# Kernel optimization log

Measured on AMD Instinct MI355X. Metric: run time of the kernel, lower is better.

The kernel has to match this reference:

```python
import jax, jax.numpy as jnp
import numpy as np

# --- config (matches init_kwargs) ---
E = 32          # n_routed_experts
G = 8           # n_group
TKG = 4         # topk_group
K = 4           # num_experts_per_tok
D = 2048        # hidden_size
H = 1024        # moe_intermediate_size
HS = 4096       # moe_shared_expert_intermediate_size
SCALE = 2.5     # routed_scaling_factor
CAP = 1024


def setup_inputs() -> dict:
    key = jax.random.key(0)
    ks = jax.random.split(key, 6)
    B, S = 2, 2048
    return dict(
        hidden_states=jax.random.normal(ks[0], (B, S, D), jnp.float32),
        gate_w=jax.random.normal(ks[1], (E, D), jnp.float32) * 0.02,
        bias_corr=jnp.zeros((E,), jnp.float32),  # e_score_correction_bias
        up_w=jax.random.normal(ks[2], (E, H, D), jnp.float32) * 0.02,
        down_w=jax.random.normal(ks[3], (E, D, H), jnp.float32) * 0.02,
        shared_up_w=jax.random.normal(ks[4], (HS, D), jnp.float32) * 0.02,
        shared_down_w=jax.random.normal(ks[5], (D, HS), jnp.float32) * 0.02,
    )


def relu2(x):
    r = jnp.maximum(x, 0.0)
    return r * r


def route_tokens(scores, bias_corr):
    # scores: sigmoid(router_logits), [T, E]
    T = scores.shape[0]
    scores_c = scores + bias_corr                                  # for choice
    group_scores = jax.lax.top_k(scores_c.reshape(T, G, E // G), 2)[0].sum(-1)  # [T, G]
    _, group_idx = jax.lax.top_k(group_scores, TKG)                # [T, TKG]
    group_mask = jnp.zeros((T, G), scores.dtype).at[jnp.arange(T)[:, None], group_idx].set(1.0)
    score_mask = jnp.repeat(group_mask, E // G, axis=1)            # [T, E]
    masked = jnp.where(score_mask > 0, scores_c, 0.0)
    _, topk_idx = jax.lax.top_k(masked, K)                         # [T, K]
    topk_w = jnp.take_along_axis(scores, topk_idx, axis=1)         # weights from raw sigmoid scores
    topk_w = topk_w / (topk_w.sum(-1, keepdims=True) + 1e-20)      # norm_topk_prob
    return topk_idx, topk_w * SCALE


def reference(hidden_states, gate_w, bias_corr, up_w, down_w, shared_up_w, shared_down_w):
    B, S, _ = hidden_states.shape
    T = B * S
    flat = hidden_states.reshape(T, D)

    logits = flat @ gate_w.T                                       # [T, E]
    scores = jax.nn.sigmoid(logits)
    topk_idx, topk_w = route_tokens(scores, bias_corr)             # [T, K] each

    # --- capacity-based dispatch (equivalent to per-expert gather + index_add combine) ---
    e_flat = topk_idx.reshape(-1)                                  # [T*K]
    oh = jax.nn.one_hot(e_flat, E, dtype=jnp.int32)                # [T*K, E]
    pos = jnp.take_along_axis(jnp.cumsum(oh, axis=0) - 1, e_flat[:, None], axis=1)[:, 0]
    tok = jnp.repeat(jnp.arange(T), K)                             # token idx per assignment
    valid = pos < CAP

    xe = jnp.zeros((E, CAP, D), flat.dtype).at[e_flat, pos].set(flat[tok], mode='drop')
    h = relu2(jnp.einsum('ecd,ehd->ech', xe, up_w))                # [E, CAP, H]
    ye = jnp.einsum('ech,edh->ecd', h, down_w)                     # [E, CAP, D]

    gathered = ye[e_flat, jnp.minimum(pos, CAP - 1)]               # [T*K, D]
    gathered = jnp.where(valid[:, None], gathered, 0.0) * topk_w.reshape(-1)[:, None]
    routed = gathered.reshape(T, K, D).sum(axis=1).reshape(B, S, D)

    shared = relu2(hidden_states @ shared_up_w.T) @ shared_down_w.T
    return routed + shared
```

## Files before the change

kernel.cpp:

```cpp
#include <hip/hip_runtime.h>

#define NE 32
#define NG 8
#define NK 4
#define ND 2048
#define NH 1024
#define NHS 4096
#define CAPE 1024
#define NT 4096

typedef float f32x4 __attribute__((ext_vector_type(4)));
typedef short s16x8 __attribute__((ext_vector_type(8)));

__device__ __forceinline__ short f2bf(float f) {
    return __builtin_bit_cast(short, (__bf16)f);
}
__device__ __forceinline__ float bf2f(short h) {
    return __builtin_bit_cast(float, ((unsigned)(unsigned short)h) << 16);
}

__device__ __forceinline__ void gload_lds16(const void* g, void* l) {
    __builtin_amdgcn_global_load_lds(
        (const __attribute__((address_space(1))) void*)g,
        (__attribute__((address_space(3))) void*)l, 16, 0, 0);
}

__global__ __launch_bounds__(256) void gate_kernel(
    const float* __restrict__ X, const float* __restrict__ Gw,
    const float* __restrict__ bias,
    int* __restrict__ topk_idx, float* __restrict__ topk_w)
{
    const int lane = threadIdx.x & 63;
    const int t = blockIdx.x * 4 + (threadIdx.x >> 6);
    const float* x = X + (size_t)t * ND;

    float xr[32];
#pragma unroll
    for (int i = 0; i < 32; i++) xr[i] = x[lane + i * 64];

    float scores[32];
#pragma unroll
    for (int e = 0; e < 32; e++) {
        const float* w = Gw + (size_t)e * ND;
        float a = 0.f;
#pragma unroll
        for (int i = 0; i < 32; i++) a = fmaf(xr[i], w[lane + i * 64], a);
#pragma unroll
        for (int s = 32; s > 0; s >>= 1) a += __shfl_xor(a, s);
        scores[e] = 1.0f / (1.0f + expf(-a));
    }

    float sc_c[32];
#pragma unroll
    for (int e = 0; e < 32; e++) sc_c[e] = scores[e] + bias[e];

    float gs[8];
#pragma unroll
    for (int g = 0; g < 8; g++) {
        float a = sc_c[4 * g], b = sc_c[4 * g + 1], c = sc_c[4 * g + 2], d = sc_c[4 * g + 3];
        float hi1 = fmaxf(a, b), lo1 = fminf(a, b);
        float hi2 = fmaxf(c, d), lo2 = fminf(c, d);
        float m1 = fmaxf(hi1, hi2);
        float m2 = fmaxf(fminf(hi1, hi2), fmaxf(lo1, lo2));
        gs[g] = m1 + m2;
    }

    unsigned gsel = 0;
#pragma unroll
    for (int it = 0; it < 4; it++) {
        int best = -1; float bv = -1e30f;
#pragma unroll
        for (int g = 0; g < 8; g++) {
            bool avail = !((gsel >> g) & 1);
            if (avail && gs[g] > bv) { bv = gs[g]; best = g; }
        }
        gsel |= 1u << best;
    }

    unsigned esel = 0;
    int idxs[4]; float wts[4];
#pragma unroll
    for (int it = 0; it < 4; it++) {
        int best = -1; float bv = -1e30f, braw = 0.f;
#pragma unroll
        for (int e = 0; e < 32; e++) {
            float mv = ((gsel >> (e >> 2)) & 1) ? sc_c[e] : 0.0f;
            bool avail = !((esel >> e) & 1);
            if (avail && mv > bv) { bv = mv; best = e; braw = scores[e]; }
        }
        esel |= 1u << best;
        idxs[it] = best; wts[it] = braw;
    }

    float s = wts[0] + wts[1] + wts[2] + wts[3] + 1e-20f;
    if (lane == 0) {
#pragma unroll
        for (int k = 0; k < 4; k++) {
            topk_idx[t * 4 + k] = idxs[k];
            topk_w[t * 4 + k] = wts[k] / s * 2.5f;
        }
    }
}

__global__ void zero_cnt(int* cnt) {
    if (threadIdx.x < NE) cnt[threadIdx.x] = 0;
}

__global__ void dispatch_kernel(const int* __restrict__ topk_idx,
                                int* __restrict__ cnt,
                                int* __restrict__ tok_list,
                                int* __restrict__ pos_list)
{
    int i = blockIdx.x * 256 + threadIdx.x;
    int e = topk_idx[i];
    int t = i >> 2;
    int pos = atomicAdd(&cnt[e], 1);
    pos_list[i] = pos;
    if (pos < CAPE) {
        tok_list[e * CAPE + pos] = t;
    }
}

__global__ __launch_bounds__(256) void cvt_f2bf(const float* __restrict__ in,
                                                short* __restrict__ out, int n8)
{
    int i = blockIdx.x * 256 + threadIdx.x;
    int stride = gridDim.x * 256;
    for (; i < n8; i += stride) {
        const f32x4* p = (const f32x4*)(in + (size_t)i * 8);
        f32x4 a = p[0], b = p[1];
        s16x8 h;
        h[0] = f2bf(a[0]); h[1] = f2bf(a[1]); h[2] = f2bf(a[2]); h[3] = f2bf(a[3]);
        h[4] = f2bf(b[0]); h[5] = f2bf(b[1]); h[6] = f2bf(b[2]); h[7] = f2bf(b[3]);
        *(s16x8*)(out + (size_t)i * 8) = h;
    }
}

__global__ __launch_bounds__(256) void combine_kernel(
    const int* __restrict__ topk_idx, const float* __restrict__ topk_w,
    const int* __restrict__ pos_list,
    const short* __restrict__ Ybuf, float* __restrict__ out)
{
    const int t = blockIdx.x;
    const int d0 = threadIdx.x * 8;

    int e[NK], p[NK]; float w[NK];
#pragma unroll
    for (int k = 0; k < NK; k++) {
        e[k] = topk_idx[t * NK + k];
        p[k] = pos_list[t * NK + k];
        w[k] = topk_w[t * NK + k];
    }

    float* orow = out + (size_t)t * ND + d0;
    f32x4 o0 = *(f32x4*)(orow);
    f32x4 o1 = *(f32x4*)(orow + 4);

#pragma unroll
    for (int k = 0; k < NK; k++) {
        if (p[k] < CAPE) {
            s16x8 y = *(const s16x8*)(Ybuf + ((size_t)e[k] * CAPE + p[k]) * ND + d0);
            o0[0] = fmaf(w[k], bf2f(y[0]), o0[0]);
            o0[1] = fmaf(w[k], bf2f(y[1]), o0[1]);
            o0[2] = fmaf(w[k], bf2f(y[2]), o0[2]);
            o0[3] = fmaf(w[k], bf2f(y[3]), o0[3]);
            o1[0] = fmaf(w[k], bf2f(y[4]), o1[0]);
            o1[1] = fmaf(w[k], bf2f(y[5]), o1[1]);
            o1[2] = fmaf(w[k], bf2f(y[6]), o1[2]);
            o1[3] = fmaf(w[k], bf2f(y[7]), o1[3]);
        }
    }
    *(f32x4*)(orow) = o0;
    *(f32x4*)(orow + 4) = o1;
}

template <int MODE, int BM, int BN>
__global__ __launch_bounds__(512, 2) void moe_gemm8(
    const short* __restrict__ Abase, const short* __restrict__ Bbase,
    const int* __restrict__ cnt, const int* __restrict__ tok_list,
    short* __restrict__ Hout, float* __restrict__ out)
{
    constexpr int K = (MODE == 0) ? ND : (MODE == 1) ? NH : (MODE == 2) ? ND : NHS;
    constexpr int NTILES = K / 64;
    constexpr int MF = BM / 32;
    constexpr int NF = BN / 64;
    constexpr int A_OPS = BM / 64;
    constexpr int B_OPS = BN / 64;
    constexpr int LOADS = A_OPS + B_OPS;

    const int e = blockIdx.z;
    const int m0 = blockIdx.y * BM, n0 = blockIdx.x * BN;

    int mcnt = 0;
    if constexpr (MODE == 0 || MODE == 1) {
        mcnt = min(cnt[e], CAPE);
        if (m0 >= mcnt) return;
    }

    __shared__ short As[2][BM * 64];
    __shared__ short Bs[2][BN * 64];

    const int tid = threadIdx.x;
    const int lane = tid & 63;
    const int wave = tid >> 6;
    const int wrM = wave >> 2;
    const int wrN = wave & 3;

    const short* Ab = Abase;
    const short* Bb = Bbase;
    if constexpr (MODE == 0) Bb += (size_t)e * NH * ND;
    if constexpr (MODE == 1) { Ab += (size_t)e * CAPE * NH; Bb += (size_t)e * ND * NH; }

    const int srow = tid >> 3;
    const int p = tid & 7;
    const int gcol = (p ^ (srow & 7)) * 8;
    const short* asrc[A_OPS];
    const short* bsrc[B_OPS];
    int dstA[A_OPS], dstB[B_OPS];
#pragma unroll
    for (int o = 0; o < A_OPS; o++) {
        int r = o * 64 + srow;
        if constexpr (MODE == 0) {
            int gr = min(m0 + r, mcnt - 1);
            int tok = tok_list[e * CAPE + gr];
            asrc[o] = Abase + (size_t)tok * ND + gcol;
        } else if constexpr (MODE == 1) {
            int gr = min(m0 + r, mcnt - 1);
            asrc[o] = Ab + (size_t)gr * NH + gcol;
        } else if constexpr (MODE == 2) {
            asrc[o] = Abase + (size_t)(m0 + r) * ND + gcol;
        } else {
            asrc[o] = Abase + (size_t)(m0 + r) * NHS + gcol;
        }
        dstA[o] = o * 4096 + wave * 512;
    }
#pragma unroll
    for (int o = 0; o < B_OPS; o++) {
        bsrc[o] = Bb + (size_t)(n0 + o * 64 + srow) * K + gcol;
        dstB[o] = o * 4096 + wave * 512;
    }

    auto STAGE = [&](int tt) {
        const int ko = (tt < NTILES ? tt : NTILES - 1) * 64;
        short* Ad = As[tt & 1];
        short* Bd = Bs[tt & 1];
#pragma unroll
        for (int o = 0; o < A_OPS; o++) gload_lds16(asrc[o] + ko, Ad + dstA[o]);
#pragma unroll
        for (int o = 0; o < B_OPS; o++) gload_lds16(bsrc[o] + ko, Bd + dstB[o]);
    };

    const int r16 = lane & 15, hi4 = lane >> 4, lo3 = lane & 7;
    const int physbase = (hi4 ^ lo3) * 8;
    int offA[MF], offB[NF];
#pragma unroll
    for (int m = 0; m < MF; m++)
        offA[m] = (wrM * (BM / 2) + m * 16 + r16) * 64 + physbase;
#pragma unroll
    for (int n = 0; n < NF; n++)
        offB[n] = (wrN * (BN / 4) + n * 16 + r16) * 64 + physbase;

    f32x4 acc[MF][NF] = {};

    STAGE(0);
    STAGE(1);

    for (int t = 0; t < NTILES; ++t) {
        const short* At = As[t & 1];
        const short* Bt = Bs[t & 1];
        if constexpr (LOADS == 6)
            asm volatile("s_waitcnt vmcnt(6)" ::: "memory");
        else if constexpr (LOADS == 8)
            asm volatile("s_waitcnt vmcnt(8)" ::: "memory");
        else
            asm volatile("s_waitcnt vmcnt(0)" ::: "memory");
        __builtin_amdgcn_s_barrier();
        __builtin_amdgcn_sched_barrier(0);
        s16x8 af[MF], bf[NF];
#pragma unroll
        for (int m = 0; m < MF; m++) af[m] = *(const s16x8*)(At + offA[m]);
#pragma unroll
        for (int n = 0; n < NF; n++) bf[n] = *(const s16x8*)(Bt + offB[n]);
        asm volatile("s_waitcnt lgkmcnt(0)" ::: "memory");
        __builtin_amdgcn_sched_barrier(0);
        __builtin_amdgcn_s_setprio(1);
#pragma unroll
        for (int m = 0; m < MF; m++)
#pragma unroll
            for (int n = 0; n < NF; n++)
                acc[m][n] = __builtin_amdgcn_mfma_f32_16x16x32_bf16(af[m], bf[n], acc[m][n], 0, 0, 0);
        __builtin_amdgcn_s_setprio(0);
        s16x8 ag[MF], bg[NF];
#pragma unroll
        for (int m = 0; m < MF; m++) ag[m] = *(const s16x8*)(At + (offA[m] ^ 32));
#pragma unroll
        for (int n = 0; n < NF; n++) bg[n] = *(const s16x8*)(Bt + (offB[n] ^ 32));
        asm volatile("s_waitcnt lgkmcnt(0)" ::: "memory");
        __builtin_amdgcn_sched_barrier(0);
        __builtin_amdgcn_s_barrier();
        __builtin_amdgcn_sched_barrier(0);
        STAGE(t + 2);
        __builtin_amdgcn_s_setprio(1);
#pragma unroll
        for (int m = 0; m < MF; m++)
#pragma unroll
            for (int n = 0; n < NF; n++)
                acc[m][n] = __builtin_amdgcn_mfma_f32_16x16x32_bf16(ag[m], bg[n], acc[m][n], 0, 0, 0);
        __builtin_amdgcn_s_setprio(0);
    }

    const int r0 = (lane >> 4) * 4;
    const int cc = lane & 15;

    if constexpr (MODE == 0 || MODE == 2) {
#pragma unroll
        for (int i = 0; i < MF; i++)
#pragma unroll
            for (int j = 0; j < NF; j++)
#pragma unroll
                for (int v = 0; v < 4; v++) {
                    int row = wrM * (BM / 2) + i * 16 + r0 + v;
                    int col = wrN * (BN / 4) + j * 16 + cc;
                    float val = acc[i][j][v];
                    float r = fmaxf(val, 0.f);
                    val = r * r;
                    if constexpr (MODE == 0)
                        Hout[((size_t)e * CAPE + m0 + row) * NH + (n0 + col)] = f2bf(val);
                    else
                        Hout[(size_t)(m0 + row) * NHS + (n0 + col)] = f2bf(val);
                }
    } else if constexpr (MODE == 3) {
#pragma unroll
        for (int i = 0; i < MF; i++)
#pragma unroll
            for (int j = 0; j < NF; j++)
#pragma unroll
                for (int v = 0; v < 4; v++) {
                    int row = wrM * (BM / 2) + i * 16 + r0 + v;
                    int col = wrN * (BN / 4) + j * 16 + cc;
                    out[(size_t)(m0 + row) * ND + (n0 + col)] = acc[i][j][v];
                }
    } else {
#pragma unroll
        for (int i = 0; i < MF; i++)
#pragma unroll
            for (int v = 0; v < 4; v++) {
                int row = wrM * (BM / 2) + i * 16 + r0 + v;
                int grow = m0 + row;
                if (grow < mcnt) {
#pragma unroll
                    for (int j = 0; j < NF; j++) {
                        int col = wrN * (BN / 4) + j * 16 + cc;
                        Hout[((size_t)e * CAPE + grow) * ND + (n0 + col)] = f2bf(acc[i][j][v]);
                    }
                }
            }
    }
}

extern "C" void kernel_launch(void* const* d_in, const int* in_sizes, int n_in,
                              void* d_out, int out_size, void* d_ws, size_t ws_size,
                              hipStream_t stream) {
    const float* X    = (const float*)d_in[0];
    const float* Gw   = (const float*)d_in[1];
    const float* bias = (const float*)d_in[2];
    const float* up_w = (const float*)d_in[3];
    const float* dn_w = (const float*)d_in[4];
    const float* sup  = (const float*)d_in[5];
    const float* sdn  = (const float*)d_in[6];
    float* out = (float*)d_out;

    char* ws = (char*)d_ws;
    size_t off = 0;
    auto alloc = [&](size_t bytes) -> void* {
        off = (off + 255) & ~(size_t)255;
        void* p = ws + off;
        off += bytes;
        return p;
    };
    int*   cnt      = (int*)  alloc(NE * 4);
    int*   topk_idx = (int*)  alloc((size_t)NT * NK * 4);
    float* topk_w   = (float*)alloc((size_t)NT * NK * 4);
    int*   pos_list = (int*)  alloc((size_t)NT * NK * 4);
    int*   tok_list = (int*)  alloc((size_t)NE * CAPE * 4);
    short* Hbuf     = (short*)alloc((size_t)NE * CAPE * NH * 2);
    short* Sbuf     = (short*)alloc((size_t)NT * NHS * 2);
    short* Xbf      = (short*)alloc((size_t)NT * ND * 2);
    short* up_bf    = (short*)alloc((size_t)NE * NH * ND * 2);
    short* dn_bf    = (short*)alloc((size_t)NE * ND * NH * 2);
    short* sup_bf   = (short*)alloc((size_t)NHS * ND * 2);
    short* sdn_bf   = (short*)alloc((size_t)ND * NHS * 2);
    short* Ybuf     = Xbf;

    gate_kernel<<<dim3(NT / 4), dim3(256), 0, stream>>>(X, Gw, bias, topk_idx, topk_w);
    zero_cnt<<<dim3(1), dim3(64), 0, stream>>>(cnt);
    dispatch_kernel<<<dim3(NT * NK / 256), dim3(256), 0, stream>>>(
        topk_idx, cnt, tok_list, pos_list);

    cvt_f2bf<<<dim3(1024), dim3(256), 0, stream>>>(X,    Xbf,    NT * ND / 8);
    cvt_f2bf<<<dim3(2048), dim3(256), 0, stream>>>(up_w, up_bf,  NE * NH * ND / 8);
    cvt_f2bf<<<dim3(2048), dim3(256), 0, stream>>>(dn_w, dn_bf,  NE * ND * NH / 8);
    cvt_f2bf<<<dim3(1024), dim3(256), 0, stream>>>(sup,  sup_bf, NHS * ND / 8);
    cvt_f2bf<<<dim3(1024), dim3(256), 0, stream>>>(sdn,  sdn_bf, ND * NHS / 8);

    moe_gemm8<0, 128, 256><<<dim3(NH / 256, CAPE / 128, NE), dim3(512), 0, stream>>>(
        Xbf, up_bf, cnt, tok_list, Hbuf, nullptr);
    moe_gemm8<2, 256, 256><<<dim3(NHS / 256, NT / 256, 1), dim3(512), 0, stream>>>(
        Xbf, sup_bf, nullptr, nullptr, Sbuf, nullptr);
    moe_gemm8<3, 256, 128><<<dim3(ND / 128, NT / 256, 1), dim3(512), 0, stream>>>(
        Sbuf, sdn_bf, nullptr, nullptr, nullptr, out);
    moe_gemm8<1, 128, 256><<<dim3(ND / 256, CAPE / 128, NE), dim3(512), 0, stream>>>(
        Hbuf, dn_bf, cnt, tok_list, Ybuf, nullptr);
    combine_kernel<<<dim3(NT), dim3(256), 0, stream>>>(
        topk_idx, topk_w, pos_list, Ybuf, out);
}
```

Measured before the change: 790.1 us.

## Use four-stage BK=32 LDS pipeline and 256-row tiles for expert GEMMs

Rewrites the GEMM main loop from a double-buffered K=64 tile with two barriers per iteration into a four-buffer ring of K=32 tiles. Loads run three stages ahead and each iteration needs only one barrier. The LDS swizzle is reworked for the 32-column row layout. The expert up/down GEMMs also move from 128-row to 256-row tiles, which halves the number of M blocks per expert. The intent is to hide more global-load latency and cut barrier overhead. In exchange, each iteration does less MFMA work, and the larger expert tiles waste more work on partially filled experts and may reduce occupancy.

```diff
diff --git a/kernel.cpp b/kernel.cpp
--- a/kernel.cpp
+++ b/kernel.cpp
@@ -181,11 +181,11 @@
     short* __restrict__ Hout, float* __restrict__ out)
 {
     constexpr int K = (MODE == 0) ? ND : (MODE == 1) ? NH : (MODE == 2) ? ND : NHS;
-    constexpr int NTILES = K / 64;
+    constexpr int NTILES = K / 32;
     constexpr int MF = BM / 32;
     constexpr int NF = BN / 64;
-    constexpr int A_OPS = BM / 64;
-    constexpr int B_OPS = BN / 64;
+    constexpr int A_OPS = BM / 128;
+    constexpr int B_OPS = BN / 128;
     constexpr int LOADS = A_OPS + B_OPS;
 
     const int e = blockIdx.z;
@@ -197,8 +197,8 @@
         if (m0 >= mcnt) return;
     }
 
-    __shared__ short As[2][BM * 64];
-    __shared__ short Bs[2][BN * 64];
+    __shared__ short As[4][BM * 32];
+    __shared__ short Bs[4][BN * 32];
 
     const int tid = threadIdx.x;
     const int lane = tid & 63;
@@ -211,15 +211,16 @@
     if constexpr (MODE == 0) Bb += (size_t)e * NH * ND;
     if constexpr (MODE == 1) { Ab += (size_t)e * CAPE * NH; Bb += (size_t)e * ND * NH; }
 
-    const int srow = tid >> 3;
-    const int p = tid & 7;
-    const int gcol = (p ^ (srow & 7)) * 8;
+    const int srow = tid >> 2;
+    const int p = tid & 3;
+    const int swzs = (srow ^ (srow >> 2)) & 3;
+    const int gcol = (p ^ swzs) * 8;
     const short* asrc[A_OPS];
     const short* bsrc[B_OPS];
     int dstA[A_OPS], dstB[B_OPS];
 #pragma unroll
     for (int o = 0; o < A_OPS; o++) {
-        int r = o * 64 + srow;
+        int r = o * 128 + srow;
         if constexpr (MODE == 0) {
             int gr = min(m0 + r, mcnt - 1);
             int tok = tok_list[e * CAPE + gr];
@@ -236,51 +237,58 @@
     }
 #pragma unroll
     for (int o = 0; o < B_OPS; o++) {
-        bsrc[o] = Bb + (size_t)(n0 + o * 64 + srow) * K + gcol;
+        bsrc[o] = Bb + (size_t)(n0 + o * 128 + srow) * K + gcol;
         dstB[o] = o * 4096 + wave * 512;
     }
 
     auto STAGE = [&](int tt) {
-        const int ko = (tt < NTILES ? tt : NTILES - 1) * 64;
-        short* Ad = As[tt & 1];
-        short* Bd = Bs[tt & 1];
+        const int ko = (tt < NTILES ? tt : NTILES - 1) * 32;
+        short* Ad = As[tt & 3];
+        short* Bd = Bs[tt & 3];
 #pragma unroll
         for (int o = 0; o < A_OPS; o++) gload_lds16(asrc[o] + ko, Ad + dstA[o]);
 #pragma unroll
         for (int o = 0; o < B_OPS; o++) gload_lds16(bsrc[o] + ko, Bd + dstB[o]);
     };
 
-    const int r16 = lane & 15, hi4 = lane >> 4, lo3 = lane & 7;
-    const int physbase = (hi4 ^ lo3) * 8;
+    const int r16 = lane & 15;
+    const int kslot = lane >> 4;
+    const int rswz = (r16 ^ (r16 >> 2)) & 3;
+    const int physcol = (kslot ^ rswz) * 8;
     int offA[MF], offB[NF];
 #pragma unroll
     for (int m = 0; m < MF; m++)
-        offA[m] = (wrM * (BM / 2) + m * 16 + r16) * 64 + physbase;
+        offA[m] = (wrM * (BM / 2) + m * 16 + r16) * 32 + physcol;
 #pragma unroll
     for (int n = 0; n < NF; n++)
-        offB[n] = (wrN * (BN / 4) + n * 16 + r16) * 64 + physbase;
+        offB[n] = (wrN * (BN / 4) + n * 16 + r16) * 32 + physcol;
 
     f32x4 acc[MF][NF] = {};
 
-    STAGE(0);
-    STAGE(1);
+    STAGE(0); STAGE(1); STAGE(2);
 
     for (int t = 0; t < NTILES; ++t) {
-        const short* At = As[t & 1];
-        const short* Bt = Bs[t & 1];
-        if constexpr (LOADS == 6)
+        const short* At = As[t & 3];
+        const short* Bt = Bs[t & 3];
+        if constexpr (LOADS == 4)
+            asm volatile("s_waitcnt vmcnt(8)" ::: "memory");
+        else if constexpr (LOADS == 3)
             asm volatile("s_waitcnt vmcnt(6)" ::: "memory");
-        else if constexpr (LOADS == 8)
-            asm volatile("s_waitcnt vmcnt(8)" ::: "memory");
+        else if constexpr (LOADS == 2)
+            asm volatile("s_waitcnt vmcnt(4)" ::: "memory");
         else
             asm volatile("s_waitcnt vmcnt(0)" ::: "memory");
         __builtin_amdgcn_s_barrier();
         __builtin_amdgcn_sched_barrier(0);
+
         s16x8 af[MF], bf[NF];
 #pragma unroll
         for (int m = 0; m < MF; m++) af[m] = *(const s16x8*)(At + offA[m]);
 #pragma unroll
         for (int n = 0; n < NF; n++) bf[n] = *(const s16x8*)(Bt + offB[n]);
+
+        STAGE(t + 3);
+
         asm volatile("s_waitcnt lgkmcnt(0)" ::: "memory");
         __builtin_amdgcn_sched_barrier(0);
         __builtin_amdgcn_s_setprio(1);
@@ -289,23 +297,6 @@
 #pragma unroll
             for (int n = 0; n < NF; n++)
                 acc[m][n] = __builtin_amdgcn_mfma_f32_16x16x32_bf16(af[m], bf[n], acc[m][n], 0, 0, 0);
-        __builtin_amdgcn_s_setprio(0);
-        s16x8 ag[MF], bg[NF];
-#pragma unroll
-        for (int m = 0; m < MF; m++) ag[m] = *(const s16x8*)(At + (offA[m] ^ 32));
-#pragma unroll
-        for (int n = 0; n < NF; n++) bg[n] = *(const s16x8*)(Bt + (offB[n] ^ 32));
-        asm volatile("s_waitcnt lgkmcnt(0)" ::: "memory");
-        __builtin_amdgcn_sched_barrier(0);
-        __builtin_amdgcn_s_barrier();
-        __builtin_amdgcn_sched_barrier(0);
-        STAGE(t + 2);
-        __builtin_amdgcn_s_setprio(1);
-#pragma unroll
-        for (int m = 0; m < MF; m++)
-#pragma unroll
-            for (int n = 0; n < NF; n++)
-                acc[m][n] = __builtin_amdgcn_mfma_f32_16x16x32_bf16(ag[m], bg[n], acc[m][n], 0, 0, 0);
         __builtin_amdgcn_s_setprio(0);
     }
 
@@ -403,13 +394,13 @@
     cvt_f2bf<<<dim3(1024), dim3(256), 0, stream>>>(sup,  sup_bf, NHS * ND / 8);
     cvt_f2bf<<<dim3(1024), dim3(256), 0, stream>>>(sdn,  sdn_bf, ND * NHS / 8);
 
-    moe_gemm8<0, 128, 256><<<dim3(NH / 256, CAPE / 128, NE), dim3(512), 0, stream>>>(
+    moe_gemm8<0, 256, 256><<<dim3(NH / 256, CAPE / 256, NE), dim3(512), 0, stream>>>(
         Xbf, up_bf, cnt, tok_list, Hbuf, nullptr);
     moe_gemm8<2, 256, 256><<<dim3(NHS / 256, NT / 256, 1), dim3(512), 0, stream>>>(
         Xbf, sup_bf, nullptr, nullptr, Sbuf, nullptr);
     moe_gemm8<3, 256, 128><<<dim3(ND / 128, NT / 256, 1), dim3(512), 0, stream>>>(
         Sbuf, sdn_bf, nullptr, nullptr, nullptr, out);
-    moe_gemm8<1, 128, 256><<<dim3(ND / 256, CAPE / 128, NE), dim3(512), 0, stream>>>(
+    moe_gemm8<1, 256, 256><<<dim3(ND / 256, CAPE / 256, NE), dim3(512), 0, stream>>>(
         Hbuf, dn_bf, cnt, tok_list, Ybuf, nullptr);
     combine_kernel<<<dim3(NT), dim3(256), 0, stream>>>(
         topk_idx, topk_w, pos_list, Ybuf, out);
```

Measured after the change: 731.6 us. 1.08x faster.
